# Kernel optimization log

Hardware: AMD Instinct MI355X
Metric: run time of the kernel (lower is better)

## Reference

```python
import jax, jax.numpy as jnp
import numpy as np

D_MODEL = 1024
N_HEADS = 16
D_HEAD = D_MODEL // N_HEADS


def setup_inputs() -> dict:
    key = jax.random.key(0)
    k1, k2, k3 = jax.random.split(key, 3)
    B, T = 2, 2048
    x = jax.random.normal(k1, (B, T, D_MODEL), dtype=jnp.float32)
    # Linear weights stored as (in, out), equivalent to torch W^T
    w_qkv = jax.random.normal(k2, (D_MODEL, 3 * D_MODEL), dtype=jnp.float32) * (D_MODEL ** -0.5)
    w_proj = jax.random.normal(k3, (D_MODEL, D_MODEL), dtype=jnp.float32) * (D_MODEL ** -0.5)
    return {"x": x, "w_qkv": w_qkv, "w_proj": w_proj}


def reference(x, w_qkv, w_proj):
    B, T, C = x.shape
    qkv = x @ w_qkv                                   # (B, T, 3C)
    qkv = qkv.reshape(B, T, 3, N_HEADS, D_HEAD)
    q, k, v = qkv[:, :, 0], qkv[:, :, 1], qkv[:, :, 2]  # (B, T, H, dh)
    q = q.transpose(0, 2, 1, 3)                        # (B, H, T, dh)
    k = k.transpose(0, 2, 1, 3)
    v = v.transpose(0, 2, 1, 3)
    scale = 1.0 / jnp.sqrt(jnp.float32(D_HEAD))
    scores = jnp.einsum('bhqd,bhkd->bhqk', q, k) * scale  # (B, H, T, T)
    causal = jnp.tril(jnp.ones((T, T), dtype=bool))
    scores = jnp.where(causal, scores, jnp.float32(-jnp.inf))
    w = jax.nn.softmax(scores, axis=-1)
    ctx = jnp.einsum('bhqk,bhkd->bhqd', w, v)          # (B, H, T, dh)
    ctx = ctx.transpose(0, 2, 1, 3).reshape(B, T, C)
    return ctx @ w_proj
```

## Files before the change

### kernel.cpp

```cpp
#include <hip/hip_runtime.h>
#include <hip/hip_bf16.h>
#include <math.h>
#include <stdint.h>

#define D_MODEL 1024
#define NHEADS  16
#define DHEAD   64
#define BATCH   2
#define SEQ     2048
#define ROWS    (BATCH*SEQ)

#define NEG_BIG (-1e30f)
#define QSCALE  0.18033688011112042f

typedef __bf16 bf16v8 __attribute__((ext_vector_type(8)));
typedef short  shortv8 __attribute__((ext_vector_type(8)));
typedef short  shortv4 __attribute__((ext_vector_type(4)));
typedef float  floatv4 __attribute__((ext_vector_type(4)));
typedef unsigned short ush;

__device__ __forceinline__ ush f2b(float f) {
  return __builtin_bit_cast(ush, (__bf16)f);
}

__device__ __forceinline__ void async16(ush* lds, const ush* g) {
  __builtin_amdgcn_global_load_lds(
      (const __attribute__((address_space(1))) void*)g,
      (__attribute__((address_space(3))) void*)lds, 16, 0, 0);
}

__global__ void detect_dtype(const uint32_t* __restrict__ x, int* __restrict__ flag) {
  if (threadIdx.x == 0 && blockIdx.x == 0) {
    int cnt = 0;
    for (int i = 0; i < 64; ++i) {
      uint32_t e = (x[i] >> 7) & 0xFF;
      cnt += (e >= 96 && e <= 144) ? 1 : 0;
    }
    *flag = (cnt >= 32) ? 1 : 0;
  }
}

__global__ __launch_bounds__(256)
void cast_to_bf16(const void* __restrict__ xin, ush* __restrict__ xb,
                  const int* __restrict__ flag) {
  int i = blockIdx.x * 256 + threadIdx.x;
  if (*flag) {
    ((shortv8*)xb)[i] = ((const shortv8*)xin)[i];
  } else {
    const floatv4* p = ((const floatv4*)xin) + (size_t)i * 2;
    floatv4 a = p[0], b = p[1];
    shortv8 o;
#pragma unroll
    for (int j = 0; j < 4; ++j) { o[j] = (short)f2b(a[j]); o[4+j] = (short)f2b(b[j]); }
    ((shortv8*)xb)[i] = o;
  }
}

__global__ __launch_bounds__(256)
void transpose_to_bf16T(const void* __restrict__ W, ush* __restrict__ Wt,
                        const int* __restrict__ flag, int K, int N) {
  __shared__ __align__(16) ush tile[64][72];
  int tiles_n = N >> 6;
  int tk = blockIdx.x / tiles_n;
  int tn = blockIdx.x % tiles_n;
  int t  = threadIdx.x;
  int r  = t >> 2;
  int c8 = (t & 3) * 8;
  int isbf = *flag;

  if (isbf) {
    const ush* src = (const ush*)W + (size_t)(tk*64 + r) * N + tn*64;
#pragma unroll
    for (int c = 0; c < 2; ++c)
      *(shortv8*)&tile[r][c8 + c*32] = *(const shortv8*)&src[c8 + c*32];
  } else {
    const float* src = (const float*)W + (size_t)(tk*64 + r) * N + tn*64;
#pragma unroll
    for (int c = 0; c < 2; ++c) {
      const floatv4* p = (const floatv4*)&src[c8 + c*32];
      floatv4 a = p[0], b = p[1];
      shortv8 o;
#pragma unroll
      for (int j = 0; j < 4; ++j) { o[j] = (short)f2b(a[j]); o[4+j] = (short)f2b(b[j]); }
      *(shortv8*)&tile[r][c8 + c*32] = o;
    }
  }
  __syncthreads();
  ush* dst = Wt + (size_t)(tn*64 + r) * K + tk*64;
#pragma unroll
  for (int c = 0; c < 2; ++c) {
    int k8 = c8 + c*32;
    shortv8 v;
#pragma unroll
    for (int j = 0; j < 8; ++j) v[j] = (short)tile[k8 + j][r];
    *(shortv8*)&dst[k8] = v;
  }
}

#define GEMM_PROLOG(Aq, Bq)                                                 \
  __shared__ __align__(16) ush smem[16384];                                 \
  const int K = 1024;                                                       \
  int bid = blockIdx.x;                                                     \
  int m0 = (bid / tiles_n) * 128;                                           \
  int n0 = (bid % tiles_n) * 128;                                           \
  int t    = threadIdx.x;                                                   \
  int lane = t & 63;                                                        \
  int w    = t >> 6;                                                        \
  int wm   = (w >> 1) * 64;                                                 \
  int wn   = (w & 1) * 64;                                                  \
  int lr   = lane & 15;                                                     \
  int quad = lane >> 4;                                                     \
  floatv4 acc[4][4] = {};                                                   \
  int r16 = lane >> 2;                                                      \
  int g4  = (lane & 3) ^ (r16 & 3);                                         \
  const ush* gA0 = Aq + (size_t)(m0 + 32*w + r16)*K + g4*8;                 \
  const ush* gA1 = gA0 + (size_t)16*K;                                      \
  const ush* gB0 = Bq + (size_t)(n0 + 32*w + r16)*K + g4*8;                 \
  const ush* gB1 = gB0 + (size_t)16*K;                                      \
  int fs = (quad ^ (lr & 3)) * 8;                                           \
  async16(&smem[(32*w)*32], gA0);                                           \
  async16(&smem[(32*w+16)*32], gA1);                                        \
  async16(&smem[8192 + (32*w)*32], gB0);                                    \
  async16(&smem[8192 + (32*w+16)*32], gB1);                                 \
  for (int kk = 0; kk < K; kk += 32) {                                      \
    int cur = (kk >> 5) & 1;                                                \
    __syncthreads();                                                        \
    if (kk + 32 < K) {                                                      \
      int nx = cur ^ 1;                                                     \
      async16(&smem[nx*4096 + (32*w)*32], gA0 + kk + 32);                   \
      async16(&smem[nx*4096 + (32*w+16)*32], gA1 + kk + 32);                \
      async16(&smem[8192 + nx*4096 + (32*w)*32], gB0 + kk + 32);            \
      async16(&smem[8192 + nx*4096 + (32*w+16)*32], gB1 + kk + 32);         \
    }                                                                       \
    bf16v8 af[4], bfr[4];                                                   \
    _Pragma("unroll")                                                       \
    for (int i = 0; i < 4; ++i) {                                           \
      af[i]  = *(bf16v8*)&smem[cur*4096 + (wm + i*16 + lr)*32 + fs];        \
      bfr[i] = *(bf16v8*)&smem[8192 + cur*4096 + (wn + i*16 + lr)*32 + fs]; \
    }                                                                       \
    _Pragma("unroll")                                                       \
    for (int i = 0; i < 4; ++i)                                             \
      _Pragma("unroll")                                                     \
      for (int j = 0; j < 4; ++j)                                           \
        acc[i][j] = __builtin_amdgcn_mfma_f32_16x16x32_bf16(bfr[i], af[j],  \
                                                            acc[i][j], 0, 0, 0); \
  }

__global__ __launch_bounds__(256, 3)
void gemm_qkv(const ush* __restrict__ A, const ush* __restrict__ Bt,
              ush* __restrict__ qb_, ush* __restrict__ kb_, ush* __restrict__ vb_,
              int tiles_n) {
  GEMM_PROLOG(A, Bt)

  int nwb = n0 + wn;
  int s   = nwb >> 10;
  int h   = (nwb & 1023) >> 6;
  int b   = (m0 + wm) >> 11;
  int bh  = b*16 + h;
  int ttw = (m0 + wm) & 2047;

  __syncthreads();

  if (s < 2) {
    ush* dst = (s == 0) ? qb_ : kb_;
    float sc = (s == 0) ? QSCALE : 1.0f;
#pragma unroll
    for (int i = 0; i < 4; ++i) {
      int d4 = i*16 + quad*4;
#pragma unroll
      for (int j = 0; j < 4; ++j) {
        int tt = ttw + j*16 + lr;
        shortv4 v4;
#pragma unroll
        for (int r = 0; r < 4; ++r) v4[r] = (short)f2b(acc[i][j][r] * sc);
        *(shortv4*)&dst[((size_t)bh*SEQ + tt)*64 + d4] = v4;
      }
    }
  } else {
    ush* L = &smem[w*4096];
#pragma unroll
    for (int i = 0; i < 4; ++i) {
#pragma unroll
      for (int r = 0; r < 4; ++r) {
        int dl = i*16 + quad*4 + r;
        shortv4 p4;
#pragma unroll
        for (int j = 0; j < 4; ++j) p4[j] = (short)f2b(acc[i][j][r]);
        int slot = (lr >> 1) ^ (dl & 7);
        *(shortv4*)&L[dl*64 + slot*8 + (lr & 1)*4] = p4;
      }
    }
#pragma unroll
    for (int p = 0; p < 8; ++p) {
      int dl = p*8 + (lane >> 3);
      int c8 = lane & 7;
      int slot = c8 ^ (dl & 7);
      shortv8 v = *(shortv8*)&L[dl*64 + slot*8];
      *(shortv8*)&vb_[((size_t)bh*64 + dl)*SEQ + ttw + c8*8] = v;
    }
  }
}

__global__ __launch_bounds__(256, 4)
void gemm_bt(const ush* __restrict__ A, const ush* __restrict__ Bt,
             void* __restrict__ Cp, const int* __restrict__ flag,
             int ldc, int tiles_n) {
  __shared__ __align__(16) ush smem[12288];
  const int K = 1024;
  int bid = blockIdx.x;
  int m0 = (bid / tiles_n) * 64;
  int n0 = (bid % tiles_n) * 128;
  int t    = threadIdx.x;
  int lane = t & 63;
  int w    = t >> 6;
  int wm   = (w >> 1) * 32;
  int wn   = (w & 1) * 64;
  int lr   = lane & 15;
  int quad = lane >> 4;
  floatv4 acc[4][2] = {};
  int r16 = lane >> 2;
  int g4  = (lane & 3) ^ (r16 & 3);
  const ush* gA0 = A  + (size_t)(m0 + 16*w + r16)*K + g4*8;
  const ush* gB0 = Bt + (size_t)(n0 + 32*w + r16)*K + g4*8;
  const ush* gB1 = gB0 + (size_t)16*K;
  int fs = (quad ^ (lr & 3)) * 8;

  async16(&smem[(16*w)*32], gA0);
  async16(&smem[4096 + (32*w)*32], gB0);
  async16(&smem[4096 + (32*w+16)*32], gB1);

  for (int kk = 0; kk < K; kk += 32) {
    int cur = (kk >> 5) & 1;
    __syncthreads();
    if (kk + 32 < K) {
      int nx = cur ^ 1;
      async16(&smem[nx*2048 + (16*w)*32], gA0 + kk + 32);
      async16(&smem[4096 + nx*4096 + (32*w)*32], gB0 + kk + 32);
      async16(&smem[4096 + nx*4096 + (32*w+16)*32], gB1 + kk + 32);
    }
    bf16v8 af[2], bfr[4];
#pragma unroll
    for (int j = 0; j < 2; ++j)
      af[j] = *(bf16v8*)&smem[cur*2048 + (wm + j*16 + lr)*32 + fs];
#pragma unroll
    for (int i = 0; i < 4; ++i)
      bfr[i] = *(bf16v8*)&smem[4096 + cur*4096 + (wn + i*16 + lr)*32 + fs];
#pragma unroll
    for (int i = 0; i < 4; ++i)
#pragma unroll
      for (int j = 0; j < 2; ++j)
        acc[i][j] = __builtin_amdgcn_mfma_f32_16x16x32_bf16(bfr[i], af[j],
                                                            acc[i][j], 0, 0, 0);
  }

  int f32out = (flag != nullptr) && (*flag == 0);
  if (f32out) {
    float* Cf = (float*)Cp;
#pragma unroll
    for (int i = 0; i < 4; ++i) {
      int nb = n0 + wn + i*16 + quad*4;
#pragma unroll
      for (int j = 0; j < 2; ++j) {
        int row = m0 + wm + j*16 + lr;
        *(floatv4*)&Cf[(size_t)row*ldc + nb] = acc[i][j];
      }
    }
  } else {
    __hip_bfloat16* Cb = (__hip_bfloat16*)Cp;
#pragma unroll
    for (int i = 0; i < 4; ++i) {
      int nb = n0 + wn + i*16 + quad*4;
#pragma unroll
      for (int j = 0; j < 2; ++j) {
        int row = m0 + wm + j*16 + lr;
        shortv4 v4;
#pragma unroll
        for (int r = 0; r < 4; ++r) v4[r] = (short)f2b(acc[i][j][r]);
        *(shortv4*)&((ush*)Cb)[(size_t)row*ldc + nb] = v4;
      }
    }
  }
}

#define PSTR 72
#define MFMA16(a,b,c) __builtin_amdgcn_mfma_f32_16x16x32_bf16(a,b,c,0,0,0)

__device__ __forceinline__ void softpack(const floatv4* s, int qw, int kb0,
                                         bool diag, ush* PsW, int quad, int lr) {
  if (diag) {
#pragma unroll
    for (int r = 0; r < 4; ++r) {
      int qv = qw + quad*4 + r;
      shortv4 p4;
#pragma unroll
      for (int j = 0; j < 4; ++j) {
        float z = (kb0 + 16*j + lr > qv) ? NEG_BIG : s[j][r];
        p4[j] = (short)f2b(__builtin_amdgcn_exp2f(z));
      }
      *(shortv4*)&PsW[(quad*4 + r)*PSTR + lr*4] = p4;
    }
  } else {
#pragma unroll
    for (int r = 0; r < 4; ++r) {
      shortv4 p4;
#pragma unroll
      for (int j = 0; j < 4; ++j)
        p4[j] = (short)f2b(__builtin_amdgcn_exp2f(s[j][r]));
      *(shortv4*)&PsW[(quad*4 + r)*PSTR + lr*4] = p4;
    }
  }
}

__global__ __launch_bounds__(512, 4)
void attn_fwd(const ush* __restrict__ qb_, const ush* __restrict__ kb_,
              const ush* __restrict__ vb_, __hip_bfloat16* __restrict__ ctx) {
  __shared__ __align__(16) ush Ks[2][64*64];
  __shared__ __align__(16) ush Vt[2][64*64];
  __shared__ __align__(16) ush Ps[8][16*PSTR];

  int bid = blockIdx.x;
  int p   = bid & 15;
  int h   = (bid >> 4) & 15;
  int b   = bid >> 8;
  int bh  = b*16 + h;

  int t = threadIdx.x, w8 = t >> 6, lane = t & 63, lr = lane & 15, quad = lane >> 4;
  int isB = w8 >> 2;
  int w   = w8 & 3;

  const ush* qh = qb_ + (size_t)bh * SEQ * 64;
  const ush* kh = kb_ + (size_t)bh * SEQ * 64;
  const ush* vh = vb_ + (size_t)bh * 64 * SEQ;

  int qt = isB ? (31 - p) : p;
  int qw = qt*64 + w*16;

  const ush* qp = qh + (size_t)(qw + lr)*64;
  bf16v8 qf0 = *(const bf16v8*)&qp[quad*8];
  bf16v8 qf1 = *(const bf16v8*)&qp[32 + quad*8];

  floatv4 acc[4] = {}, acl = {};

  bf16v8 ones;
#pragma unroll
  for (int j = 0; j < 8; ++j) ones[j] = (__bf16)1.0f;

  int r8 = lane >> 3;
  int s8 = lane & 7;
  int g8 = s8 ^ r8;
  const ush* kg = kh + (size_t)(8*w8 + r8)*64 + g8*8;
  const ush* vg = vh + (size_t)(8*w8 + r8)*SEQ + g8*8;
  int lo = (8*w8)*64;

  int sl0 = quad ^ (lr & 7);
  int sl1 = (quad + 4) ^ (lr & 7);

  int ntiles = 32 - p;

  async16(&Ks[0][lo], kg);
  async16(&Vt[0][lo], vg);

  for (int tk = 0; tk < ntiles; ++tk) {
    int cur = tk & 1;
    __syncthreads();
    if (tk + 1 < ntiles) {
      int nx = cur ^ 1;
      async16(&Ks[nx][lo], kg + (size_t)(tk + 1) * 64 * 64);
      async16(&Vt[nx][lo], vg + (size_t)(tk + 1) * 64);
    }

    bool live = isB | (tk <= p);
    if (live) {
      int kb0 = tk * 64;
      bool diag = (tk == qt);

      floatv4 s[4] = {};
#pragma unroll
      for (int j = 0; j < 4; ++j) {
        if (!diag || j <= w) {
          int row = 16*j + lr;
          bf16v8 kf0 = *(bf16v8*)&Ks[cur][row*64 + sl0*8];
          bf16v8 kf1 = *(bf16v8*)&Ks[cur][row*64 + sl1*8];
          s[j] = MFMA16(qf0, kf0, s[j]);
          s[j] = MFMA16(qf1, kf1, s[j]);
        }
      }

      softpack(s, qw, kb0, diag, &Ps[w8][0], quad, lr);

      bf16v8 pf0 = *(bf16v8*)&Ps[w8][lr*PSTR + quad*8];
      bf16v8 pf1 = *(bf16v8*)&Ps[w8][lr*PSTR + 32 + quad*8];
      acl = MFMA16(pf0, ones, acl);
      acl = MFMA16(pf1, ones, acl);

#pragma unroll
      for (int c = 0; c < 4; ++c) {
        int row = 16*c + lr;
        bf16v8 vf0 = *(bf16v8*)&Vt[cur][row*64 + sl0*8];
        bf16v8 vf1 = *(bf16v8*)&Vt[cur][row*64 + sl1*8];
        acc[c] = MFMA16(pf0, vf0, acc[c]);
        acc[c] = MFMA16(pf1, vf1, acc[c]);
      }
    }
  }

#pragma unroll
  for (int r = 0; r < 4; ++r) {
    float inv = 1.0f / fmaxf(acl[r], 1e-30f);
    size_t o = (size_t)(b*SEQ + qw + quad*4 + r) * D_MODEL + h*64;
#pragma unroll
    for (int c = 0; c < 4; ++c)
      ctx[o + c*16 + lr] = __float2bfloat16(acc[c][r] * inv);
  }
}

extern "C" void kernel_launch(void* const* d_in, const int* in_sizes, int n_in,
                              void* d_out, int out_size, void* d_ws, size_t ws_size,
                              hipStream_t stream) {
  const void* x      = d_in[0];
  const void* w_qkv  = d_in[1];
  const void* w_proj = d_in[2];

  int* flag   = (int*)d_ws;
  ush* xb     = (ush*)d_ws + 8;
  ush* wqkvT  = xb     + (size_t)ROWS * D_MODEL;
  ush* wprojT = wqkvT  + (size_t)3072 * 1024;
  ush* qbuf   = wprojT + (size_t)1024 * 1024;
  ush* kbuf   = qbuf   + (size_t)32 * SEQ * 64;
  ush* vbuf   = kbuf   + (size_t)32 * SEQ * 64;
  ush* ctx    = xb;

  detect_dtype<<<1, 64, 0, stream>>>((const uint32_t*)x, flag);

  cast_to_bf16<<<(ROWS*D_MODEL/8)/256, 256, 0, stream>>>(x, xb, flag);

  transpose_to_bf16T<<<(1024/64)*(3072/64), 256, 0, stream>>>(w_qkv,  wqkvT, flag, 1024, 3072);
  transpose_to_bf16T<<<(1024/64)*(1024/64), 256, 0, stream>>>(w_proj, wprojT, flag, 1024, 1024);

  gemm_qkv<<<(ROWS/128)*(3072/128), 256, 0, stream>>>(
      xb, wqkvT, qbuf, kbuf, vbuf, 3072/128);

  attn_fwd<<<BATCH * NHEADS * 16, 512, 0, stream>>>(
      qbuf, kbuf, vbuf, (__hip_bfloat16*)ctx);

  gemm_bt<<<(ROWS/64)*(1024/128), 256, 0, stream>>>(
      ctx, wprojT, d_out, flag, 1024, 1024/128);
}
```

Baseline: 195.8 us.

## Fuse dtype detect, cast and weight transposes into one prep kernel; add setprio

```diff
diff --git a/kernel.cpp b/kernel.cpp
--- a/kernel.cpp
+++ b/kernel.cpp
@@ -29,71 +29,76 @@
       (__attribute__((address_space(3))) void*)lds, 16, 0, 0);
 }
 
-__global__ void detect_dtype(const uint32_t* __restrict__ x, int* __restrict__ flag) {
-  if (threadIdx.x == 0 && blockIdx.x == 0) {
-    int cnt = 0;
-    for (int i = 0; i < 64; ++i) {
-      uint32_t e = (x[i] >> 7) & 0xFF;
-      cnt += (e >= 96 && e <= 144) ? 1 : 0;
-    }
-    *flag = (cnt >= 32) ? 1 : 0;
-  }
-}
-
 __global__ __launch_bounds__(256)
-void cast_to_bf16(const void* __restrict__ xin, ush* __restrict__ xb,
-                  const int* __restrict__ flag) {
-  int i = blockIdx.x * 256 + threadIdx.x;
-  if (*flag) {
-    ((shortv8*)xb)[i] = ((const shortv8*)xin)[i];
-  } else {
-    const floatv4* p = ((const floatv4*)xin) + (size_t)i * 2;
-    floatv4 a = p[0], b = p[1];
-    shortv8 o;
-#pragma unroll
-    for (int j = 0; j < 4; ++j) { o[j] = (short)f2b(a[j]); o[4+j] = (short)f2b(b[j]); }
-    ((shortv8*)xb)[i] = o;
-  }
-}
-
-__global__ __launch_bounds__(256)
-void transpose_to_bf16T(const void* __restrict__ W, ush* __restrict__ Wt,
-                        const int* __restrict__ flag, int K, int N) {
+void prep(const uint32_t* __restrict__ x, ush* __restrict__ xb,
+          const void* __restrict__ wqkv, ush* __restrict__ wqkvT,
+          const void* __restrict__ wproj, ush* __restrict__ wprojT,
+          int* __restrict__ flagp) {
+  __shared__ int sflag;
   __shared__ __align__(16) ush tile[64][72];
-  int tiles_n = N >> 6;
-  int tk = blockIdx.x / tiles_n;
-  int tn = blockIdx.x % tiles_n;
-  int t  = threadIdx.x;
-  int r  = t >> 2;
-  int c8 = (t & 3) * 8;
-  int isbf = *flag;
-
-  if (isbf) {
-    const ush* src = (const ush*)W + (size_t)(tk*64 + r) * N + tn*64;
-#pragma unroll
-    for (int c = 0; c < 2; ++c)
-      *(shortv8*)&tile[r][c8 + c*32] = *(const shortv8*)&src[c8 + c*32];
-  } else {
-    const float* src = (const float*)W + (size_t)(tk*64 + r) * N + tn*64;
-#pragma unroll
-    for (int c = 0; c < 2; ++c) {
-      const floatv4* p = (const floatv4*)&src[c8 + c*32];
+
+  int bid = blockIdx.x;
+  int t   = threadIdx.x;
+
+  if (t < 64) {
+    uint32_t e = (x[t] >> 7) & 0xFF;
+    unsigned long long m = __ballot(e >= 96 && e <= 144);
+    if (t == 0) sflag = (__popcll(m) >= 32) ? 1 : 0;
+  }
+  __syncthreads();
+  int isbf = sflag;
+  if (bid == 0 && t == 0) *flagp = isbf;
+
+  if (bid < 2048) {
+    size_t i = (size_t)bid * 256 + t;
+    if (isbf) {
+      ((shortv8*)xb)[i] = ((const shortv8*)x)[i];
+    } else {
+      const floatv4* p = ((const floatv4*)x) + i * 2;
       floatv4 a = p[0], b = p[1];
       shortv8 o;
 #pragma unroll
       for (int j = 0; j < 4; ++j) { o[j] = (short)f2b(a[j]); o[4+j] = (short)f2b(b[j]); }
-      *(shortv8*)&tile[r][c8 + c*32] = o;
-    }
-  }
-  __syncthreads();
-  ush* dst = Wt + (size_t)(tn*64 + r) * K + tk*64;
-#pragma unroll
-  for (int c = 0; c < 2; ++c) {
-    int k8 = c8 + c*32;
-    shortv8 v;
-#pragma unroll
-    for (int j = 0; j < 8; ++j) v[j] = (short)tile[k8 + j][r];
-    *(shortv8*)&dst[k8] = v;
+      ((shortv8*)xb)[i] = o;
+    }
+  } else {
+    const void* W; ush* Wt; int N, b2;
+    const int K = 1024;
+    if (bid < 2816) { W = wqkv;  Wt = wqkvT;  N = 3072; b2 = bid - 2048; }
+    else            { W = wproj; Wt = wprojT; N = 1024; b2 = bid - 2816; }
+    int tiles_n = N >> 6;
+    int tk = b2 / tiles_n;
+    int tn = b2 % tiles_n;
+    int r  = t >> 2;
+    int c8 = (t & 3) * 8;
+
+    if (isbf) {
+      const ush* src = (const ush*)W + (size_t)(tk*64 + r) * N + tn*64;
+#pragma unroll
+      for (int c = 0; c < 2; ++c)
+        *(shortv8*)&tile[r][c8 + c*32] = *(const shortv8*)&src[c8 + c*32];
+    } else {
+      const float* src = (const float*)W + (size_t)(tk*64 + r) * N + tn*64;
+#pragma unroll
+      for (int c = 0; c < 2; ++c) {
+        const floatv4* p = (const floatv4*)&src[c8 + c*32];
+        floatv4 a = p[0], b = p[1];
+        shortv8 o;
+#pragma unroll
+        for (int j = 0; j < 4; ++j) { o[j] = (short)f2b(a[j]); o[4+j] = (short)f2b(b[j]); }
+        *(shortv8*)&tile[r][c8 + c*32] = o;
+      }
+    }
+    __syncthreads();
+    ush* dst = Wt + (size_t)(tn*64 + r) * K + tk*64;
+#pragma unroll
+    for (int c = 0; c < 2; ++c) {
+      int k8 = c8 + c*32;
+      shortv8 v;
+#pragma unroll
+      for (int j = 0; j < 8; ++j) v[j] = (short)tile[k8 + j][r];
+      *(shortv8*)&dst[k8] = v;
+    }
   }
 }
 
@@ -375,6 +380,7 @@
       bool diag = (tk == qt);
 
       floatv4 s[4] = {};
+      __builtin_amdgcn_s_setprio(1);
 #pragma unroll
       for (int j = 0; j < 4; ++j) {
         if (!diag || j <= w) {
@@ -385,11 +391,14 @@
           s[j] = MFMA16(qf1, kf1, s[j]);
         }
       }
+      __builtin_amdgcn_s_setprio(0);
 
       softpack(s, qw, kb0, diag, &Ps[w8][0], quad, lr);
 
       bf16v8 pf0 = *(bf16v8*)&Ps[w8][lr*PSTR + quad*8];
       bf16v8 pf1 = *(bf16v8*)&Ps[w8][lr*PSTR + 32 + quad*8];
+
+      __builtin_amdgcn_s_setprio(1);
       acl = MFMA16(pf0, ones, acl);
       acl = MFMA16(pf1, ones, acl);
 
@@ -401,6 +410,7 @@
         acc[c] = MFMA16(pf0, vf0, acc[c]);
         acc[c] = MFMA16(pf1, vf1, acc[c]);
       }
+      __builtin_amdgcn_s_setprio(0);
     }
   }
 
@@ -430,12 +440,8 @@
   ush* vbuf   = kbuf   + (size_t)32 * SEQ * 64;
   ush* ctx    = xb;
 
-  detect_dtype<<<1, 64, 0, stream>>>((const uint32_t*)x, flag);
-
-  cast_to_bf16<<<(ROWS*D_MODEL/8)/256, 256, 0, stream>>>(x, xb, flag);
-
-  transpose_to_bf16T<<<(1024/64)*(3072/64), 256, 0, stream>>>(w_qkv,  wqkvT, flag, 1024, 3072);
-  transpose_to_bf16T<<<(1024/64)*(1024/64), 256, 0, stream>>>(w_proj, wprojT, flag, 1024, 1024);
+  prep<<<3072, 256, 0, stream>>>((const uint32_t*)x, xb,
+                                 w_qkv, wqkvT, w_proj, wprojT, flag);
 
   gemm_qkv<<<(ROWS/128)*(3072/128), 256, 0, stream>>>(
       xb, wqkvT, qbuf, kbuf, vbuf, 3072/128);
```

After: 190.2 us. 1.03x faster.
